# Optimization experiments

Measured on AMD Instinct MI355X. Metric: run time of the kernel, lower is better.

Reference implementation:

```python
import jax, jax.numpy as jnp
import numpy as np

EPS = 1e-6  # F.pairwise_distance default eps, added to the difference


def setup_inputs() -> dict:
    key = jax.random.key(0)
    k1, k2 = jax.random.split(key)
    N, NS, NQ, D = 2048, 5, 8, 256
    x = jax.random.normal(k1, (N, NS + NQ, D), dtype=jnp.float32)
    label = jax.random.randint(k2, (N,), 0, N, dtype=jnp.int64)
    return {"x": x, "label": label, "n_s": NS, "n_q": NQ}


def reference(x, label, n_s, n_q):
    # x: [N, n_s+n_q, D]
    anchors = jnp.mean(x[:, :n_s, :], axis=1)               # [N, D] prototypes
    N, D = anchors.shape
    queries = x[:, n_s:n_s + n_q, :].reshape(N * n_q, D)     # [N*n_q, D]

    # Exact ||q - a + eps||^2 via GEMM expansion (matches F.pairwise_distance(.,.)**2):
    # ||q-a||^2 + 2*eps*sum(q-a) + D*eps^2
    q_sq = jnp.sum(queries * queries, axis=-1)               # [N*n_q]
    a_sq = jnp.sum(anchors * anchors, axis=-1)               # [N]
    cross = queries @ anchors.T                              # [N*n_q, N]
    q_sum = jnp.sum(queries, axis=-1)                        # [N*n_q]
    a_sum = jnp.sum(anchors, axis=-1)                        # [N]
    dist_sq = (q_sq[:, None] + a_sq[None, :] - 2.0 * cross
               + 2.0 * EPS * (q_sum[:, None] - a_sum[None, :])
               + D * EPS * EPS)
    logits = -dist_sq                                        # [N*n_q, N]

    lab = jnp.repeat(label, n_q)                             # [N*n_q]
    logp = jax.nn.log_softmax(logits, axis=-1)
    nloss = -jnp.mean(jnp.take_along_axis(logp, lab[:, None], axis=1))
    prec1 = jnp.mean((jnp.argmax(logits, axis=-1) == lab).astype(jnp.float32)) * 100.0
    return nloss, prec1
```

## Files before the change

kernel.cpp:

```cpp
#include <hip/hip_runtime.h>
#include <math.h>

#define EPS  1e-6f
#define DD   256
#define NSUP 5
#define NQ   8
#define SEQ  13
#define L2E  1.44269504088896f
#define LN2  0.693147180559945f
#define NEP  2048
#define NROW 16384
#define NCOL 2048

typedef short bf16x8 __attribute__((ext_vector_type(8)));
typedef unsigned short u16x4 __attribute__((ext_vector_type(4)));
typedef float f32x4  __attribute__((ext_vector_type(4)));

__device__ __forceinline__ ushort f2bf(float f) {
  union { float f; unsigned u; } v; v.f = f;
  unsigned r = v.u + 0x7FFFu + ((v.u >> 16) & 1u);
  return (ushort)(r >> 16);
}
__device__ __forceinline__ float bf2f(short u) {
  union { unsigned u; float f; } v; v.u = ((unsigned)(unsigned short)u) << 16;
  return v.f;
}

__global__ __launch_bounds__(256) void proto_prep(
    const float* __restrict__ x, float* __restrict__ cb,
    ushort* __restrict__ Asw, ushort* __restrict__ Qsw,
    float* __restrict__ accum, int* __restrict__ fincount) {
  const int tid = threadIdx.x, g = tid >> 6, l = tid & 63;
  const int n = blockIdx.x * 4 + g;
  if (blockIdx.x == 0 && tid == 0) { accum[0] = 0.f; accum[1] = 0.f; fincount[0] = 0; }

  const float4* xr4 = (const float4*)(x + (size_t)n * SEQ * DD);

  const int d0   = l * 4;
  const int kk   = d0 >> 5, quad = (d0 >> 3) & 3, j = d0 & 7;
  const size_t chunk_d = (size_t)kk * 64 + (size_t)quad * 16;

  float4 a = {0.f, 0.f, 0.f, 0.f};
  #pragma unroll
  for (int s = 0; s < NSUP; ++s) {
    float4 v = xr4[s * 64 + l];
    a.x += v.x; a.y += v.y; a.z += v.z; a.w += v.w;
  }
  a.x *= 0.2f; a.y *= 0.2f; a.z *= 0.2f; a.w *= 0.2f;
  {
    const size_t idx = (((size_t)(n >> 4) * 8) * 64 + chunk_d + (n & 15)) * 8 + j;
    u16x4 o = {f2bf(a.x), f2bf(a.y), f2bf(a.z), f2bf(a.w)};
    *(u16x4*)(Asw + idx) = o;
  }
  float s1 = a.x + a.y + a.z + a.w;
  float s2 = a.x * a.x + a.y * a.y + a.z * a.z + a.w * a.w;
  #pragma unroll
  for (int off = 32; off; off >>= 1) {
    s1 += __shfl_xor(s1, off);
    s2 += __shfl_xor(s2, off);
  }
  if (l == 0) cb[n] = -L2E * (s2 - 2.f * EPS * s1);

  #pragma unroll
  for (int s = 0; s < NQ; ++s) {
    float4 q = xr4[(NSUP + s) * 64 + l];
    const int row = n * NQ + s;
    const size_t idx = (((size_t)(row >> 4) * 8) * 64 + chunk_d + (row & 15)) * 8 + j;
    u16x4 o = {f2bf(q.x), f2bf(q.y), f2bf(q.z), f2bf(q.w)};
    *(u16x4*)(Qsw + idx) = o;
  }
}

__global__ __launch_bounds__(512, 2) void proto_main(
    const ushort* __restrict__ Qsw, const ushort* __restrict__ Asw,
    const float* __restrict__ cb, const int* __restrict__ label,
    float* __restrict__ accum, int* __restrict__ fincount,
    float* __restrict__ out) {
  const int tid  = threadIdx.x;
  const int wid  = tid >> 6, lane = tid & 63;
  const int quad = lane >> 4, lcol = lane & 15;
  const int r0   = blockIdx.x * 64;

  const bf16x8* qb = (const bf16x8*)Qsw;
  const bf16x8* bb = (const bf16x8*)Asw;

  bf16x8 af[4][8];
  #pragma unroll
  for (int set = 0; set < 4; ++set) {
    const size_t base = ((size_t)((r0 >> 4) + set) * 8) * 64 + lane;
    #pragma unroll
    for (int kk = 0; kk < 8; ++kk) af[set][kk] = qb[base + (size_t)kk * 64];
  }

  float m[4][4], s[4][4];
  int   bi[4][4];
  #pragma unroll
  for (int set = 0; set < 4; ++set)
    #pragma unroll
    for (int i = 0; i < 4; ++i) {
      m[set][i] = -1e30f; s[set][i] = 0.f; bi[set][i] = 0x7fffffff;
    }

  auto process = [&](int T, bf16x8* B) {
    f32x4 c0 = {0.f, 0.f, 0.f, 0.f}, c1 = {0.f, 0.f, 0.f, 0.f};
    f32x4 c2 = {0.f, 0.f, 0.f, 0.f}, c3 = {0.f, 0.f, 0.f, 0.f};
    #pragma unroll
    for (int kk = 0; kk < 8; ++kk) {
      c0 = __builtin_amdgcn_mfma_f32_16x16x32_bf16(af[0][kk], B[kk], c0, 0, 0, 0);
      c1 = __builtin_amdgcn_mfma_f32_16x16x32_bf16(af[1][kk], B[kk], c1, 0, 0, 0);
      c2 = __builtin_amdgcn_mfma_f32_16x16x32_bf16(af[2][kk], B[kk], c2, 0, 0, 0);
      c3 = __builtin_amdgcn_mfma_f32_16x16x32_bf16(af[3][kk], B[kk], c3, 0, 0, 0);
    }
    const int   colIdx = T * 16 + lcol;
    const float cbv    = cb[colIdx];
    #pragma unroll
    for (int set = 0; set < 4; ++set) {
      #pragma unroll
      for (int i = 0; i < 4; ++i) {
        float cv = (set == 0) ? c0[i] : (set == 1) ? c1[i]
                 : (set == 2) ? c2[i] : c3[i];
        float v2 = fmaf(cv, 2.f * L2E, cbv);
        float dv = v2 - m[set][i];
        bool  gt = dv > 0.f;
        float e  = exp2f(-fabsf(dv));
        s[set][i]  = fmaf(s[set][i], gt ? e : 1.f, gt ? 1.f : e);
        m[set][i]  = fmaxf(m[set][i], v2);
        bi[set][i] = gt ? colIdx : bi[set][i];
      }
    }
  };

  const int T0 = wid * 16;
  bf16x8 buf0[8], buf1[8];
  #pragma unroll
  for (int kk = 0; kk < 8; ++kk)
    buf0[kk] = bb[((size_t)T0 * 8 + (size_t)kk) * 64 + lane];

  #pragma unroll 1
  for (int t = 0; t < 16; t += 2) {
    {
      const int Tn = T0 + t + 1;
      #pragma unroll
      for (int kk = 0; kk < 8; ++kk)
        buf1[kk] = bb[((size_t)Tn * 8 + (size_t)kk) * 64 + lane];
    }
    process(T0 + t, buf0);
    {
      const int Tm = (t + 2 < 16) ? T0 + t + 2 : T0 + t + 1;
      #pragma unroll
      for (int kk = 0; kk < 8; ++kk)
        buf0[kk] = bb[((size_t)Tm * 8 + (size_t)kk) * 64 + lane];
    }
    process(T0 + t + 1, buf1);
  }

  #pragma unroll
  for (int mask = 1; mask < 16; mask <<= 1) {
    #pragma unroll
    for (int set = 0; set < 4; ++set)
      #pragma unroll
      for (int i = 0; i < 4; ++i) {
        float om = __shfl_xor(m[set][i], mask);
        float os = __shfl_xor(s[set][i], mask);
        int   oi = __shfl_xor(bi[set][i], mask);
        float nm = fmaxf(m[set][i], om);
        s[set][i] = s[set][i] * exp2f(m[set][i] - nm) + os * exp2f(om - nm);
        bool better = (om > m[set][i]) || (om == m[set][i] && oi < bi[set][i]);
        bi[set][i] = better ? oi : bi[set][i];
        m[set][i]  = nm;
      }
  }

  __shared__ float sm[8][64], ssh[8][64], slab[64];
  __shared__ int   sbi[8][64];
  if (lcol == 0) {
    #pragma unroll
    for (int set = 0; set < 4; ++set)
      #pragma unroll
      for (int i = 0; i < 4; ++i) {
        int rl = set * 16 + quad * 4 + i;
        sm[wid][rl] = m[set][i]; ssh[wid][rl] = s[set][i]; sbi[wid][rl] = bi[set][i];
      }
  }

  {
    const int rl = tid >> 3, l = tid & 7;
    const int row = r0 + rl;
    const int lab = label[row >> 3];
    const int kk  = l;
    float dot = 0.f;
    const size_t qc = ((size_t)(row >> 4) * 8 + kk) * 64 + (row & 15);
    const size_t ac = ((size_t)(lab >> 4) * 8 + kk) * 64 + (lab & 15);
    #pragma unroll
    for (int qd = 0; qd < 4; ++qd) {
      bf16x8 qv = qb[qc + qd * 16];
      bf16x8 av = bb[ac + qd * 16];
      #pragma unroll
      for (int j = 0; j < 8; ++j) dot = fmaf(bf2f(qv[j]), bf2f(av[j]), dot);
    }
    dot += __shfl_xor(dot, 1);
    dot += __shfl_xor(dot, 2);
    dot += __shfl_xor(dot, 4);
    if (l == 0) slab[rl] = fmaf(dot, 2.f * L2E, cb[lab]);
  }
  __syncthreads();

  if (tid < 64) {
    float mm = sm[0][tid], sv = ssh[0][tid];
    int   b  = sbi[0][tid];
    #pragma unroll
    for (int w = 1; w < 8; ++w) {
      float om = sm[w][tid], os = ssh[w][tid];
      int   oi = sbi[w][tid];
      float nm = fmaxf(mm, om);
      sv = sv * exp2f(mm - nm) + os * exp2f(om - nm);
      bool better = (om > mm) || (om == mm && oi < b);
      b = better ? oi : b;
      mm = nm;
    }
    const int row = r0 + tid;
    const int lb  = label[row >> 3];
    float loss = LN2 * (mm + log2f(sv) - slab[tid]);
    float corr = (b == lb) ? 1.f : 0.f;
    #pragma unroll
    for (int mask = 32; mask; mask >>= 1) {
      loss += __shfl_xor(loss, mask);
      corr += __shfl_xor(corr, mask);
    }
    if (tid == 0) {
      atomicAdd(&accum[0], loss);
      atomicAdd(&accum[1], corr);
      __threadfence();
      if (atomicAdd(fincount, 1) == (int)gridDim.x - 1) {
        out[0] = atomicAdd(&accum[0], 0.f) / (float)NROW;
        out[1] = atomicAdd(&accum[1], 0.f) * 100.f / (float)NROW;
      }
    }
  }
}

extern "C" void kernel_launch(void* const* d_in, const int* in_sizes, int n_in,
                              void* d_out, int out_size, void* d_ws, size_t ws_size,
                              hipStream_t stream) {
  const float* x     = (const float*)d_in[0];
  const int*   label = (const int*)d_in[1];
  float* out = (float*)d_out;

  float*  W        = (float*)d_ws;
  float*  accum    = W;
  int*    fincount = (int*)(W + 2);
  float*  cb       = W + 16;
  ushort* Asw      = (ushort*)(cb + NCOL);
  ushort* Qsw      = Asw + (size_t)NCOL * DD;

  hipLaunchKernelGGL(proto_prep, dim3(NEP / 4), dim3(256), 0, stream,
                     x, cb, Asw, Qsw, accum, fincount);
  hipLaunchKernelGGL(proto_main, dim3(NROW / 64), dim3(512), 0, stream,
                     Qsw, Asw, cb, label, accum, fincount, out);
}
```

Measured before the change: 120.5 us.

## Stage anchor tiles in LDS via direct global-to-LDS loads with 16-wave blocks

Each block now runs 16 waves arranged as 4 row groups by 4 column groups. Each wave holds one 16-row query fragment instead of four, and the anchor tiles are staged cooperatively into double-buffered shared memory with global_load_lds. Every anchor tile is fetched once per column group and shared by the four row-group waves, which cuts redundant global/L2 traffic and register pressure so more waves can be resident. In exchange, each wave issues fewer MFMAs per B fragment, the loop adds two block-wide barriers per tile pair, and B operands are read from LDS.

```diff
diff --git a/kernel.cpp b/kernel.cpp
--- a/kernel.cpp
+++ b/kernel.cpp
@@ -71,7 +71,7 @@
   }
 }
 
-__global__ __launch_bounds__(512, 2) void proto_main(
+__global__ __launch_bounds__(1024, 4) void proto_main(
     const ushort* __restrict__ Qsw, const ushort* __restrict__ Asw,
     const float* __restrict__ cb, const int* __restrict__ label,
     float* __restrict__ accum, int* __restrict__ fincount,
@@ -79,111 +79,99 @@
   const int tid  = threadIdx.x;
   const int wid  = tid >> 6, lane = tid & 63;
   const int quad = lane >> 4, lcol = lane & 15;
+  const int rowg = wid & 3, colg = wid >> 2;
   const int r0   = blockIdx.x * 64;
 
   const bf16x8* qb = (const bf16x8*)Qsw;
   const bf16x8* bb = (const bf16x8*)Asw;
 
-  bf16x8 af[4][8];
-  #pragma unroll
-  for (int set = 0; set < 4; ++set) {
-    const size_t base = ((size_t)((r0 >> 4) + set) * 8) * 64 + lane;
-    #pragma unroll
-    for (int kk = 0; kk < 8; ++kk) af[set][kk] = qb[base + (size_t)kk * 64];
-  }
-
-  float m[4][4], s[4][4];
-  int   bi[4][4];
-  #pragma unroll
-  for (int set = 0; set < 4; ++set)
+  __shared__ bf16x8 Bl[4][2][8][64];
+
+  bf16x8 af[8];
+  {
+    const size_t base = ((size_t)(blockIdx.x * 4 + rowg) * 8) * 64 + lane;
+    #pragma unroll
+    for (int kk = 0; kk < 8; ++kk) af[kk] = qb[base + (size_t)kk * 64];
+  }
+
+  float m[4], s[4];
+  int   bi[4];
+  #pragma unroll
+  for (int i = 0; i < 4; ++i) { m[i] = -1e30f; s[i] = 0.f; bi[i] = 0x7fffffff; }
+
+  const int kk0 = rowg * 2;
+  auto stage = [&](int tl, int b) {
+    const int T = colg * 32 + tl;
+    #pragma unroll
+    for (int k2 = 0; k2 < 2; ++k2) {
+      const int kk = kk0 + k2;
+      const ushort* src = Asw + (((size_t)T * 8 + kk) * 64 + lane) * 8;
+      __builtin_amdgcn_global_load_lds(
+          (const __attribute__((address_space(1))) void*)src,
+          (__attribute__((address_space(3))) void*)&Bl[colg][b][kk][0],
+          16, 0, 0);
+    }
+  };
+
+  auto compute = [&](int tl, int b) {
+    f32x4 c = {0.f, 0.f, 0.f, 0.f};
+    #pragma unroll
+    for (int kk = 0; kk < 8; ++kk)
+      c = __builtin_amdgcn_mfma_f32_16x16x32_bf16(af[kk], Bl[colg][b][kk][lane],
+                                                  c, 0, 0, 0);
+    const int   colIdx = (colg * 32 + tl) * 16 + lcol;
+    const float cbv    = cb[colIdx];
     #pragma unroll
     for (int i = 0; i < 4; ++i) {
-      m[set][i] = -1e30f; s[set][i] = 0.f; bi[set][i] = 0x7fffffff;
-    }
-
-  auto process = [&](int T, bf16x8* B) {
-    f32x4 c0 = {0.f, 0.f, 0.f, 0.f}, c1 = {0.f, 0.f, 0.f, 0.f};
-    f32x4 c2 = {0.f, 0.f, 0.f, 0.f}, c3 = {0.f, 0.f, 0.f, 0.f};
-    #pragma unroll
-    for (int kk = 0; kk < 8; ++kk) {
-      c0 = __builtin_amdgcn_mfma_f32_16x16x32_bf16(af[0][kk], B[kk], c0, 0, 0, 0);
-      c1 = __builtin_amdgcn_mfma_f32_16x16x32_bf16(af[1][kk], B[kk], c1, 0, 0, 0);
-      c2 = __builtin_amdgcn_mfma_f32_16x16x32_bf16(af[2][kk], B[kk], c2, 0, 0, 0);
-      c3 = __builtin_amdgcn_mfma_f32_16x16x32_bf16(af[3][kk], B[kk], c3, 0, 0, 0);
-    }
-    const int   colIdx = T * 16 + lcol;
-    const float cbv    = cb[colIdx];
-    #pragma unroll
-    for (int set = 0; set < 4; ++set) {
-      #pragma unroll
-      for (int i = 0; i < 4; ++i) {
-        float cv = (set == 0) ? c0[i] : (set == 1) ? c1[i]
-                 : (set == 2) ? c2[i] : c3[i];
-        float v2 = fmaf(cv, 2.f * L2E, cbv);
-        float dv = v2 - m[set][i];
-        bool  gt = dv > 0.f;
-        float e  = exp2f(-fabsf(dv));
-        s[set][i]  = fmaf(s[set][i], gt ? e : 1.f, gt ? 1.f : e);
-        m[set][i]  = fmaxf(m[set][i], v2);
-        bi[set][i] = gt ? colIdx : bi[set][i];
-      }
+      float v2 = fmaf(c[i], 2.f * L2E, cbv);
+      float dv = v2 - m[i];
+      bool  gt = dv > 0.f;
+      float e  = exp2f(-fabsf(dv));
+      s[i]  = fmaf(s[i], gt ? e : 1.f, gt ? 1.f : e);
+      m[i]  = fmaxf(m[i], v2);
+      bi[i] = gt ? colIdx : bi[i];
     }
   };
 
-  const int T0 = wid * 16;
-  bf16x8 buf0[8], buf1[8];
-  #pragma unroll
-  for (int kk = 0; kk < 8; ++kk)
-    buf0[kk] = bb[((size_t)T0 * 8 + (size_t)kk) * 64 + lane];
+  stage(0, 0);
+  __syncthreads();
 
   #pragma unroll 1
-  for (int t = 0; t < 16; t += 2) {
-    {
-      const int Tn = T0 + t + 1;
-      #pragma unroll
-      for (int kk = 0; kk < 8; ++kk)
-        buf1[kk] = bb[((size_t)Tn * 8 + (size_t)kk) * 64 + lane];
-    }
-    process(T0 + t, buf0);
-    {
-      const int Tm = (t + 2 < 16) ? T0 + t + 2 : T0 + t + 1;
-      #pragma unroll
-      for (int kk = 0; kk < 8; ++kk)
-        buf0[kk] = bb[((size_t)Tm * 8 + (size_t)kk) * 64 + lane];
-    }
-    process(T0 + t + 1, buf1);
+  for (int t = 0; t < 32; t += 2) {
+    stage(t + 1, 1);
+    compute(t, 0);
+    __syncthreads();
+    if (t + 2 < 32) stage(t + 2, 0);
+    compute(t + 1, 1);
+    __syncthreads();
   }
 
   #pragma unroll
   for (int mask = 1; mask < 16; mask <<= 1) {
     #pragma unroll
-    for (int set = 0; set < 4; ++set)
-      #pragma unroll
-      for (int i = 0; i < 4; ++i) {
-        float om = __shfl_xor(m[set][i], mask);
-        float os = __shfl_xor(s[set][i], mask);
-        int   oi = __shfl_xor(bi[set][i], mask);
-        float nm = fmaxf(m[set][i], om);
-        s[set][i] = s[set][i] * exp2f(m[set][i] - nm) + os * exp2f(om - nm);
-        bool better = (om > m[set][i]) || (om == m[set][i] && oi < bi[set][i]);
-        bi[set][i] = better ? oi : bi[set][i];
-        m[set][i]  = nm;
-      }
-  }
-
-  __shared__ float sm[8][64], ssh[8][64], slab[64];
-  __shared__ int   sbi[8][64];
+    for (int i = 0; i < 4; ++i) {
+      float om = __shfl_xor(m[i], mask);
+      float os = __shfl_xor(s[i], mask);
+      int   oi = __shfl_xor(bi[i], mask);
+      float nm = fmaxf(m[i], om);
+      s[i] = s[i] * exp2f(m[i] - nm) + os * exp2f(om - nm);
+      bool better = (om > m[i]) || (om == m[i] && oi < bi[i]);
+      bi[i] = better ? oi : bi[i];
+      m[i]  = nm;
+    }
+  }
+
+  __shared__ float sm[4][64], ssh[4][64], slab[64];
+  __shared__ int   sbi[4][64];
   if (lcol == 0) {
     #pragma unroll
-    for (int set = 0; set < 4; ++set)
-      #pragma unroll
-      for (int i = 0; i < 4; ++i) {
-        int rl = set * 16 + quad * 4 + i;
-        sm[wid][rl] = m[set][i]; ssh[wid][rl] = s[set][i]; sbi[wid][rl] = bi[set][i];
-      }
-  }
-
-  {
+    for (int i = 0; i < 4; ++i) {
+      int rl = rowg * 16 + quad * 4 + i;
+      sm[colg][rl] = m[i]; ssh[colg][rl] = s[i]; sbi[colg][rl] = bi[i];
+    }
+  }
+
+  if (tid < 512) {
     const int rl = tid >> 3, l = tid & 7;
     const int row = r0 + rl;
     const int lab = label[row >> 3];
@@ -209,7 +197,7 @@
     float mm = sm[0][tid], sv = ssh[0][tid];
     int   b  = sbi[0][tid];
     #pragma unroll
-    for (int w = 1; w < 8; ++w) {
+    for (int w = 1; w < 4; ++w) {
       float om = sm[w][tid], os = ssh[w][tid];
       int   oi = sbi[w][tid];
       float nm = fmaxf(mm, om);
@@ -255,6 +243,6 @@
 
   hipLaunchKernelGGL(proto_prep, dim3(NEP / 4), dim3(256), 0, stream,
                      x, cb, Asw, Qsw, accum, fincount);
-  hipLaunchKernelGGL(proto_main, dim3(NROW / 64), dim3(512), 0, stream,
+  hipLaunchKernelGGL(proto_main, dim3(NROW / 64), dim3(1024), 0, stream,
                      Qsw, Asw, cb, label, accum, fincount, out);
 }
```

Result: no change. 120.3 us (-0.1%).

## Split row tiles across wave pairs and share anchor tiles via LDS

Applied to the files above, without the earlier changes.

Doubles the block to 16 waves. Each pair of waves now shares one column group, and each wave holds only two query row-sets in registers instead of four. Anchor tiles are staged into double-buffered LDS with global_load_lds, each wave of a pair loading half the K chunks, and block-wide barriers separate the stages. The aim is to cut register pressure so occupancy can rise and to halve redundant global anchor loads. The cost is two __syncthreads per tile step plus LDS traffic, and launch bounds of 1024 with 4 blocks may force register spills.

```diff
diff --git a/kernel.cpp b/kernel.cpp
--- a/kernel.cpp
+++ b/kernel.cpp
@@ -71,7 +71,7 @@
   }
 }
 
-__global__ __launch_bounds__(512, 2) void proto_main(
+__global__ __launch_bounds__(1024, 4) void proto_main(
     const ushort* __restrict__ Qsw, const ushort* __restrict__ Asw,
     const float* __restrict__ cb, const int* __restrict__ label,
     float* __restrict__ accum, int* __restrict__ fincount,
@@ -79,46 +79,60 @@
   const int tid  = threadIdx.x;
   const int wid  = tid >> 6, lane = tid & 63;
   const int quad = lane >> 4, lcol = lane & 15;
+  const int rowg = wid & 1, colg = wid >> 1;
   const int r0   = blockIdx.x * 64;
 
   const bf16x8* qb = (const bf16x8*)Qsw;
   const bf16x8* bb = (const bf16x8*)Asw;
 
-  bf16x8 af[4][8];
-  #pragma unroll
-  for (int set = 0; set < 4; ++set) {
-    const size_t base = ((size_t)((r0 >> 4) + set) * 8) * 64 + lane;
+  __shared__ bf16x8 Bl[8][2][8][64];
+
+  bf16x8 af[2][8];
+  #pragma unroll
+  for (int set = 0; set < 2; ++set) {
+    const size_t base = ((size_t)(blockIdx.x * 4 + rowg * 2 + set) * 8) * 64 + lane;
     #pragma unroll
     for (int kk = 0; kk < 8; ++kk) af[set][kk] = qb[base + (size_t)kk * 64];
   }
 
-  float m[4][4], s[4][4];
-  int   bi[4][4];
-  #pragma unroll
-  for (int set = 0; set < 4; ++set)
+  float m[2][4], s[2][4];
+  int   bi[2][4];
+  #pragma unroll
+  for (int set = 0; set < 2; ++set)
     #pragma unroll
     for (int i = 0; i < 4; ++i) {
       m[set][i] = -1e30f; s[set][i] = 0.f; bi[set][i] = 0x7fffffff;
     }
 
-  auto process = [&](int T, bf16x8* B) {
+  const int kk0 = rowg * 4;
+  auto stage = [&](int tl, int b) {
+    const int T = colg * 16 + tl;
+    #pragma unroll
+    for (int k2 = 0; k2 < 4; ++k2) {
+      const int kk = kk0 + k2;
+      const ushort* src = Asw + (((size_t)T * 8 + kk) * 64 + lane) * 8;
+      __builtin_amdgcn_global_load_lds(
+          (const __attribute__((address_space(1))) void*)src,
+          (__attribute__((address_space(3))) void*)&Bl[colg][b][kk][0],
+          16, 0, 0);
+    }
+  };
+
+  auto compute = [&](int tl, int b) {
     f32x4 c0 = {0.f, 0.f, 0.f, 0.f}, c1 = {0.f, 0.f, 0.f, 0.f};
-    f32x4 c2 = {0.f, 0.f, 0.f, 0.f}, c3 = {0.f, 0.f, 0.f, 0.f};
     #pragma unroll
     for (int kk = 0; kk < 8; ++kk) {
-      c0 = __builtin_amdgcn_mfma_f32_16x16x32_bf16(af[0][kk], B[kk], c0, 0, 0, 0);
-      c1 = __builtin_amdgcn_mfma_f32_16x16x32_bf16(af[1][kk], B[kk], c1, 0, 0, 0);
-      c2 = __builtin_amdgcn_mfma_f32_16x16x32_bf16(af[2][kk], B[kk], c2, 0, 0, 0);
-      c3 = __builtin_amdgcn_mfma_f32_16x16x32_bf16(af[3][kk], B[kk], c3, 0, 0, 0);
-    }
-    const int   colIdx = T * 16 + lcol;
+      bf16x8 bf = Bl[colg][b][kk][lane];
+      c0 = __builtin_amdgcn_mfma_f32_16x16x32_bf16(af[0][kk], bf, c0, 0, 0, 0);
+      c1 = __builtin_amdgcn_mfma_f32_16x16x32_bf16(af[1][kk], bf, c1, 0, 0, 0);
+    }
+    const int   colIdx = (colg * 16 + tl) * 16 + lcol;
     const float cbv    = cb[colIdx];
     #pragma unroll
-    for (int set = 0; set < 4; ++set) {
+    for (int set = 0; set < 2; ++set) {
       #pragma unroll
       for (int i = 0; i < 4; ++i) {
-        float cv = (set == 0) ? c0[i] : (set == 1) ? c1[i]
-                 : (set == 2) ? c2[i] : c3[i];
+        float cv = set ? c1[i] : c0[i];
         float v2 = fmaf(cv, 2.f * L2E, cbv);
         float dv = v2 - m[set][i];
         bool  gt = dv > 0.f;
@@ -130,34 +144,23 @@
     }
   };
 
-  const int T0 = wid * 16;
-  bf16x8 buf0[8], buf1[8];
-  #pragma unroll
-  for (int kk = 0; kk < 8; ++kk)
-    buf0[kk] = bb[((size_t)T0 * 8 + (size_t)kk) * 64 + lane];
+  stage(0, 0);
+  __syncthreads();
 
   #pragma unroll 1
   for (int t = 0; t < 16; t += 2) {
-    {
-      const int Tn = T0 + t + 1;
-      #pragma unroll
-      for (int kk = 0; kk < 8; ++kk)
-        buf1[kk] = bb[((size_t)Tn * 8 + (size_t)kk) * 64 + lane];
-    }
-    process(T0 + t, buf0);
-    {
-      const int Tm = (t + 2 < 16) ? T0 + t + 2 : T0 + t + 1;
-      #pragma unroll
-      for (int kk = 0; kk < 8; ++kk)
-        buf0[kk] = bb[((size_t)Tm * 8 + (size_t)kk) * 64 + lane];
-    }
-    process(T0 + t + 1, buf1);
+    stage(t + 1, 1);
+    compute(t, 0);
+    __syncthreads();
+    if (t + 2 < 16) stage(t + 2, 0);
+    compute(t + 1, 1);
+    __syncthreads();
   }
 
   #pragma unroll
   for (int mask = 1; mask < 16; mask <<= 1) {
     #pragma unroll
-    for (int set = 0; set < 4; ++set)
+    for (int set = 0; set < 2; ++set)
       #pragma unroll
       for (int i = 0; i < 4; ++i) {
         float om = __shfl_xor(m[set][i], mask);
@@ -175,15 +178,15 @@
   __shared__ int   sbi[8][64];
   if (lcol == 0) {
     #pragma unroll
-    for (int set = 0; set < 4; ++set)
+    for (int set = 0; set < 2; ++set)
       #pragma unroll
       for (int i = 0; i < 4; ++i) {
-        int rl = set * 16 + quad * 4 + i;
-        sm[wid][rl] = m[set][i]; ssh[wid][rl] = s[set][i]; sbi[wid][rl] = bi[set][i];
-      }
-  }
-
-  {
+        int rl = rowg * 32 + set * 16 + quad * 4 + i;
+        sm[colg][rl] = m[set][i]; ssh[colg][rl] = s[set][i]; sbi[colg][rl] = bi[set][i];
+      }
+  }
+
+  if (tid < 512) {
     const int rl = tid >> 3, l = tid & 7;
     const int row = r0 + rl;
     const int lab = label[row >> 3];
@@ -255,6 +258,6 @@
 
   hipLaunchKernelGGL(proto_prep, dim3(NEP / 4), dim3(256), 0, stream,
                      x, cb, Asw, Qsw, accum, fincount);
-  hipLaunchKernelGGL(proto_main, dim3(NROW / 64), dim3(512), 0, stream,
+  hipLaunchKernelGGL(proto_main, dim3(NROW / 64), dim3(1024), 0, stream,
                      Qsw, Asw, cb, label, accum, fincount, out);
 }
```

After: 121.8 us. Within noise of the previous version (+1.1%).
